# Kernel tuning notes

Hardware: AMD Instinct MI355X
Metric: run time of the kernel (lower is better)

Reference implementation:

```python
import jax, jax.numpy as jnp
import numpy as np

# --- dims (match init_kwargs) ---
B, IN_DIM, OUT_DIM, CAUSES_DIM = 4096, 512, 4096, 256
POOL = 2
N_STEPS = 10
GAMMA = 0.1
LR = 0.001  # fixed lr inside _IstaStep
S = int(np.sqrt(OUT_DIM))   # 64: side of the square code map
SP = S // POOL              # 32: pooled side
POOLED_DIM = SP * SP        # 1024: second dim of V (pool path)


def setup_inputs() -> dict:
    key = jax.random.key(0)
    k1, k2, k3 = jax.random.split(key, 3)
    inputs = jax.random.normal(k1, (B, IN_DIM), jnp.float32)
    limit = float(np.sqrt(6.0 / (OUT_DIM + IN_DIM)))  # glorot_uniform for W
    W = jax.random.uniform(k2, (OUT_DIM, IN_DIM), jnp.float32, -limit, limit)
    # pool_flag=True -> V ~ U(0, 1) with shape (causes_dim, pooled_dim)
    V = jax.random.uniform(k3, (CAUSES_DIM, POOLED_DIM), jnp.float32, 0.0, 1.0)
    return {"inputs": inputs, "W": W, "V": V}


def _soft_threshold(x, t):
    # _proxOp: max(x - t, 0) + min(x + t, 0)
    return jnp.maximum(x - t, 0.0) + jnp.minimum(x + t, 0.0)


def reference(inputs, W, V):
    Bn = inputs.shape[0]
    x0 = jnp.zeros((Bn, OUT_DIM), inputs.dtype)
    u0 = jnp.full((Bn, CAUSES_DIM), 0.1, inputs.dtype)   # zeros + 0.1
    rec0 = jnp.zeros((Bn, IN_DIM), inputs.dtype)

    def step(carry, _):
        x, u, _rec = carry
        outputs = x @ W                                   # [B, IN_DIM], linear activation
        # NOTE: original uses (1 + exp(-z)) * 0.5 (not a true sigmoid) — keep faithful
        causes = (1.0 + jnp.exp(-(u @ V))) * 0.5          # [B, POOLED_DIM]
        # nearest-neighbor upsample of the pooled cause map back to the code map
        causes_up = jnp.repeat(
            jnp.repeat(causes.reshape(Bn, SP, SP), POOL, axis=1), POOL, axis=2
        ).reshape(Bn, OUT_DIM)                            # [B, OUT_DIM]
        # T.grad(sum((inputs - x@W)^2), x) = 2 * (x@W - inputs) @ W.T
        grad_x = 2.0 * (outputs - inputs) @ W.T           # [B, OUT_DIM]
        # prior=0 in _get_output, so the _proxInnov branch is dead code
        x_new = jax.lax.stop_gradient(                    # disconnected_grad
            _soft_threshold(x - LR * grad_x, LR * GAMMA * causes_up))
        # 2x2 max pool over the square code map
        x_pool = x_new.reshape(Bn, SP, POOL, SP, POOL).max(axis=(2, 4)).reshape(Bn, POOLED_DIM)
        # T.grad(sum(causes(u) * x_pool * gamma), u): d causes/dz = -0.5*exp(-z)
        dcauses = -0.5 * jnp.exp(-(u @ V))                # [B, POOLED_DIM]
        grad_u = (dcauses * x_pool * GAMMA) @ V.T         # [B, CAUSES_DIM]
        u_new = jax.lax.stop_gradient(
            _soft_threshold(u - LR * grad_u, LR * GAMMA / 10.0))
        return (x_new, u_new, outputs), None

    (x, u, rec), _ = jax.lax.scan(step, (x0, u0, rec0), None, length=N_STEPS)
    # return_mode='rec': reconstruction computed in the last step (from x_{T-1})
    return rec
```

## Files before the change

kernel.cpp:

```cpp
#include <hip/hip_runtime.h>
#include <math.h>


#define NB 4096
#define IN_DIM 512
#define OUT_DIM 4096
#define CAUSES_DIM 256
#define POOLED_DIM 1024

typedef __attribute__((ext_vector_type(8))) short short8;
typedef __attribute__((ext_vector_type(4))) float f32x4;

static constexpr float LR = 0.001f;
static constexpr float GAMMA = 0.1f;

enum { EP_R = 0, EP_OUT, EP_CAUSES, EP_XUP, EP_XUP_LAST, EP_UUP };

__device__ __forceinline__ float softthr(float v, float t) {
    return fmaxf(v - t, 0.0f) + fminf(v + t, 0.0f);
}
__device__ __forceinline__ unsigned short f2bf(float f) {
    unsigned int u = __builtin_bit_cast(unsigned int, f);
    u = (u + 0x7fffu + ((u >> 16) & 1u)) >> 16;
    return (unsigned short)u;
}
__device__ __forceinline__ float bf2f(unsigned short h) {
    return __builtin_bit_cast(float, (unsigned int)h << 16);
}
__device__ __forceinline__ void gload_lds16(const unsigned short* g, unsigned short* l) {
    __builtin_amdgcn_global_load_lds(
        (const __attribute__((address_space(1))) void*)g,
        (__attribute__((address_space(3))) void*)l, 16, 0, 0);
}

template<int BM, int BN, int N, int K, int EP>
__global__ __launch_bounds__(256)
void gemm_bf16(const unsigned short* __restrict__ A, const unsigned short* __restrict__ B,
               const float* __restrict__ auxf,
               const unsigned short* __restrict__ cbf,
               const unsigned short* __restrict__ dcbf,
               void* __restrict__ out0, void* __restrict__ out1)
{
    constexpr int WM = BM / 2, WN = BN / 2;
    constexpr int FM = WM / 16, FN = WN / 16;
    constexpr int NK = K / 64;
    constexpr int NX = N / BN;
    constexpr int NWG = (NB / BM) * NX;
    constexpr bool POOLF = (EP == EP_XUP);
    constexpr int TILE = (BM + BN) * 64;
    constexpr int XS_SHORTS = 128 * 130;
    constexpr int LDS_SHORTS =
        (POOLF && XS_SHORTS > 2 * TILE) ? XS_SHORTS : 2 * TILE;
    __shared__ unsigned short lds[LDS_SHORTS];
    unsigned short* A0 = lds;
    unsigned short* B0 = lds + BM * 64;
    unsigned short* A1 = lds + TILE;
    unsigned short* B1 = lds + TILE + BM * 64;
    unsigned short* xs = lds;

    const int t    = threadIdx.x;
    const int lane = t & 63, wid = t >> 6;
    const int l15  = lane & 15, l7 = lane & 7, g = lane >> 4;
    const int work = ((blockIdx.x & 7) * (NWG / 8)) + (blockIdx.x >> 3);
    const int bn = work % NX, bm = work / NX;
    const int m0 = bm * BM, n0 = bn * BN;
    const int wm0 = (wid >> 1) * WM, wn0 = (wid & 1) * WN;

    f32x4 acc[FM][FN];
#pragma unroll
    for (int fi = 0; fi < FM; fi++)
#pragma unroll
        for (int fj = 0; fj < FN; fj++) acc[fi][fj] = (f32x4){0.f, 0.f, 0.f, 0.f};

    auto stage = [&](unsigned short* As, unsigned short* Bs, int k0) {
#pragma unroll
        for (int j = 0; j < BM / 32; j++) {
            const int idx = j * 256 + t;
            const int row = idx >> 3;
            const int sl  = (idx & 7) ^ (row & 7);
            gload_lds16(A + (size_t)(m0 + row) * K + k0 + sl * 8,
                        As + (size_t)(idx & ~63) * 8);
        }
#pragma unroll
        for (int j = 0; j < BN / 32; j++) {
            const int idx = j * 256 + t;
            const int row = idx >> 3;
            const int sl  = (idx & 7) ^ (row & 7);
            gload_lds16(B + (size_t)(n0 + row) * K + k0 + sl * 8,
                        Bs + (size_t)(idx & ~63) * 8);
        }
    };
    auto compute = [&](const unsigned short* As, const unsigned short* Bs) {
#pragma unroll
        for (int ks = 0; ks < 2; ks++) {
            const int so = (((ks * 4) + g) ^ l7) * 8;
            short8 af[FM], bfv[FN];
#pragma unroll
            for (int fi = 0; fi < FM; fi++)
                af[fi] = *(const short8*)&As[(wm0 + fi * 16 + l15) * 64 + so];
#pragma unroll
            for (int fj = 0; fj < FN; fj++)
                bfv[fj] = *(const short8*)&Bs[(wn0 + fj * 16 + l15) * 64 + so];
#pragma unroll
            for (int fi = 0; fi < FM; fi++)
#pragma unroll
                for (int fj = 0; fj < FN; fj++)
                    acc[fi][fj] = __builtin_amdgcn_mfma_f32_16x16x32_bf16(
                        af[fi], bfv[fj], acc[fi][fj], 0, 0, 0);
        }
    };

    stage(A0, B0, 0);
    __syncthreads();
#pragma unroll 1
    for (int kt = 0; kt < NK; kt += 2) {
        stage(A1, B1, (kt + 1) * 64);
        compute(A0, B0);
        __syncthreads();
        if (kt + 2 < NK) stage(A0, B0, (kt + 2) * 64);
        compute(A1, B1);
        __syncthreads();
    }

#pragma unroll
    for (int fi = 0; fi < FM; fi++) {
#pragma unroll
        for (int fj = 0; fj < FN; fj++) {
#pragma unroll
            for (int r = 0; r < 4; r++) {
                const int row = m0 + wm0 + fi * 16 + g * 4 + r;
                const int col = n0 + wn0 + fj * 16 + l15;
                const float v = acc[fi][fj][r];
                if (EP == EP_R) {
                    ((unsigned short*)out0)[(size_t)row * N + col] =
                        f2bf(v - auxf[(size_t)row * N + col]);
                } else if (EP == EP_OUT) {
                    ((float*)out0)[(size_t)row * N + col] = v;
                } else if (EP == EP_CAUSES) {
                    const float e = expf(-v);
                    ((unsigned short*)out0)[(size_t)row * N + col] = f2bf(0.5f + 0.5f * e);
                    ((unsigned short*)out1)[(size_t)row * N + col] = f2bf(-0.5f * e);
                } else if (EP == EP_XUP || EP == EP_XUP_LAST) {
                    const int pcol = (col & 63) >> 1;
                    const float cz = bf2f(cbf[(size_t)row * POOLED_DIM + bn * 32 + pcol]);
                    unsigned short* xbf = (unsigned short*)out0;
                    const size_t idx = (size_t)row * OUT_DIM + col;
                    const float xold = bf2f(xbf[idx]);
                    const float xv = softthr(xold - 2.0f * LR * v, LR * GAMMA * cz);
                    const unsigned short xq = f2bf(xv);
                    xbf[idx] = xq;
                    if (POOLF) {
                        const int rloc = wm0 + fi * 16 + g * 4 + r;
                        const int cloc = wn0 + fj * 16 + l15;
                        xs[rloc * 130 + cloc] = xq;
                    }
                } else {
                    float* up = (float*)out0;
                    const size_t idx = (size_t)row * CAUSES_DIM + col;
                    const float uv = softthr(up[idx] - LR * v, LR * GAMMA * 0.1f);
                    up[idx] = uv;
                    ((unsigned short*)out1)[idx] = f2bf(uv);
                }
            }
        }
    }

    if (POOLF) {
        __syncthreads();
        const int prow = t & 127;
        const int half = t >> 7;
        const size_t gp = (size_t)(m0 + prow) * POOLED_DIM + bn * 32 + half * 16;
        short8 dc0 = *(const short8*)&dcbf[gp];
        short8 dc1 = *(const short8*)&dcbf[gp + 8];
        unsigned short res[16];
#pragma unroll
        for (int i = 0; i < 16; i++) {
            const int pc = half * 16 + i;
            const unsigned short* xr = &xs[prow * 130 + 2 * pc];
            const float mx = fmaxf(fmaxf(bf2f(xr[0]), bf2f(xr[1])),
                                   fmaxf(bf2f(xr[64]), bf2f(xr[65])));
            const float dcv = bf2f((unsigned short)(i < 8 ? dc0[i] : dc1[i - 8]));
            res[i] = f2bf(dcv * mx * GAMMA);
        }
        unsigned short* gbf = (unsigned short*)out1;
        *(short8*)&gbf[gp]     = *(const short8*)&res[0];
        *(short8*)&gbf[gp + 8] = *(const short8*)&res[8];
    }
}

__global__ void cast_bf16_k(const float* __restrict__ in, unsigned short* __restrict__ out,
                            int n4, int neg)
{
    const int i = blockIdx.x * 256 + threadIdx.x;
    if (i >= n4) return;
    float4 v = ((const float4*)in)[i];
    if (neg) { v.x = -v.x; v.y = -v.y; v.z = -v.z; v.w = -v.w; }
    union { unsigned short s[4]; unsigned long long u; } p;
    p.s[0] = f2bf(v.x); p.s[1] = f2bf(v.y); p.s[2] = f2bf(v.z); p.s[3] = f2bf(v.w);
    ((unsigned long long*)out)[i] = p.u;
}

__global__ __launch_bounds__(256)
void transpose_cast_k(const float* __restrict__ in, unsigned short* __restrict__ out,
                      int R, int C)
{
    __shared__ float tile[32][33];
    const int bx = blockIdx.x * 32, by = blockIdx.y * 32;
    const int tx = threadIdx.x % 32, ty = threadIdx.x / 32;
#pragma unroll
    for (int i = 0; i < 32; i += 8)
        tile[ty + i][tx] = in[(size_t)(by + ty + i) * C + bx + tx];
    __syncthreads();
#pragma unroll
    for (int i = 0; i < 32; i += 8)
        out[(size_t)(bx + ty + i) * R + by + tx] = f2bf(tile[tx][ty + i]);
}

__global__ void fill_zero_u16(unsigned short* __restrict__ p, size_t n8) {
    for (size_t i = (size_t)blockIdx.x * 256 + threadIdx.x; i < n8;
         i += (size_t)gridDim.x * 256)
        ((ulonglong2*)p)[i] = (ulonglong2){0ull, 0ull};
}

__global__ void fill_u_k(float* __restrict__ u, unsigned short* __restrict__ ubf, int n) {
    const int i = blockIdx.x * 256 + threadIdx.x;
    if (i >= n) return;
    u[i] = 0.1f;
    ubf[i] = f2bf(0.1f);
}

extern "C" void kernel_launch(void* const* d_in, const int* in_sizes, int n_in,
                              void* d_out, int out_size, void* d_ws, size_t ws_size,
                              hipStream_t stream)
{
    const float* inputs = (const float*)d_in[0];
    const float* W      = (const float*)d_in[1];
    const float* V      = (const float*)d_in[2];
    float* out = (float*)d_out;

    char* w = (char*)d_ws;
    unsigned short* xbf  = (unsigned short*)w; w += (size_t)NB * OUT_DIM * 2;
    unsigned short* Rbf  = (unsigned short*)w; w += (size_t)NB * IN_DIM * 2;
    unsigned short* cbf  = (unsigned short*)w; w += (size_t)NB * POOLED_DIM * 2;
    unsigned short* dcbf = (unsigned short*)w; w += (size_t)NB * POOLED_DIM * 2;
    unsigned short* gbf  = (unsigned short*)w; w += (size_t)NB * POOLED_DIM * 2;
    float*          u    = (float*)w;          w += (size_t)NB * CAUSES_DIM * 4;
    unsigned short* ubf  = (unsigned short*)w; w += (size_t)NB * CAUSES_DIM * 2;
    unsigned short* Wbf  = (unsigned short*)w; w += (size_t)OUT_DIM * IN_DIM * 2;
    unsigned short* WTbf = (unsigned short*)w; w += (size_t)OUT_DIM * IN_DIM * 2;
    unsigned short* Vbf  = (unsigned short*)w; w += (size_t)CAUSES_DIM * POOLED_DIM * 2;
    unsigned short* VTbf = (unsigned short*)w;

    cast_bf16_k<<<OUT_DIM * IN_DIM / 4 / 256, 256, 0, stream>>>(W, Wbf, OUT_DIM * IN_DIM / 4, 0);
    cast_bf16_k<<<CAUSES_DIM * POOLED_DIM / 4 / 256, 256, 0, stream>>>(V, Vbf, CAUSES_DIM * POOLED_DIM / 4, 0);
    transpose_cast_k<<<dim3(IN_DIM / 32, OUT_DIM / 32), 256, 0, stream>>>(W, WTbf, OUT_DIM, IN_DIM);
    transpose_cast_k<<<dim3(POOLED_DIM / 32, CAUSES_DIM / 32), 256, 0, stream>>>(V, VTbf, CAUSES_DIM, POOLED_DIM);
    fill_zero_u16<<<2048, 256, 0, stream>>>(xbf, (size_t)NB * OUT_DIM / 8);
    fill_u_k<<<NB * CAUSES_DIM / 256, 256, 0, stream>>>(u, ubf, NB * CAUSES_DIM);
    cast_bf16_k<<<NB * IN_DIM / 4 / 256, 256, 0, stream>>>(inputs, Rbf, NB * IN_DIM / 4, 1);

    for (int t = 0; t < 9; t++) {
        if (t > 0) {
            gemm_bf16<64, 64, IN_DIM, OUT_DIM, EP_R><<<512, 256, 0, stream>>>(
                xbf, WTbf, inputs, nullptr, nullptr, Rbf, nullptr);
        }
        gemm_bf16<64, 64, POOLED_DIM, CAUSES_DIM, EP_CAUSES><<<1024, 256, 0, stream>>>(
            ubf, VTbf, nullptr, nullptr, nullptr, cbf, dcbf);
        if (t < 8) {
            gemm_bf16<128, 128, OUT_DIM, IN_DIM, EP_XUP><<<1024, 256, 0, stream>>>(
                Rbf, Wbf, nullptr, cbf, dcbf, xbf, gbf);
            gemm_bf16<64, 64, CAUSES_DIM, POOLED_DIM, EP_UUP><<<256, 256, 0, stream>>>(
                gbf, Vbf, nullptr, nullptr, nullptr, u, ubf);
        } else {
            gemm_bf16<128, 128, OUT_DIM, IN_DIM, EP_XUP_LAST><<<1024, 256, 0, stream>>>(
                Rbf, Wbf, nullptr, cbf, nullptr, xbf, nullptr);
        }
    }
    gemm_bf16<64, 64, IN_DIM, OUT_DIM, EP_OUT><<<512, 256, 0, stream>>>(
        xbf, WTbf, nullptr, nullptr, nullptr, out, nullptr);
}
```

Baseline: 843.2 us.

## Fuse causes GEMM into x-update kernel and co-launch R and u-update GEMMs

Computes the u@V causes tile inside the x-update kernel, so the causes and derivative values stay in LDS and the cbf/dcbf global buffers and the separate causes launch go away. The residual GEMM and the u-update GEMM are merged into one launch that dispatches on block index, which also lets them run concurrently. The residual and output GEMMs switch to 128x64 tiles. Each x-update block now redundantly computes a 128x32 slice of u@V (K=256), and the concurrent u-update reads the x written in the same step, which matches the original ordering.

```diff
diff --git a/kernel.cpp b/kernel.cpp
--- a/kernel.cpp
+++ b/kernel.cpp
@@ -14,7 +14,7 @@
 static constexpr float LR = 0.001f;
 static constexpr float GAMMA = 0.1f;
 
-enum { EP_R = 0, EP_OUT, EP_CAUSES, EP_XUP, EP_XUP_LAST, EP_UUP };
+enum { EP_R = 0, EP_OUT, EP_UUP };
 
 __device__ __forceinline__ float softthr(float v, float t) {
     return fmaxf(v - t, 0.0f) + fminf(v + t, 0.0f);
@@ -33,35 +33,41 @@
         (__attribute__((address_space(3))) void*)l, 16, 0, 0);
 }
 
+template<int ROWS, int K>
+__device__ __forceinline__ void stage_tile(const unsigned short* __restrict__ g,
+                                           unsigned short* l, int row0, int k0, int t)
+{
+#pragma unroll
+    for (int j = 0; j < ROWS / 32; j++) {
+        const int idx = j * 256 + t;
+        const int row = idx >> 3;
+        const int sl  = (idx & 7) ^ (row & 7);
+        gload_lds16(g + (size_t)(row0 + row) * K + k0 + sl * 8,
+                    l + (size_t)(idx & ~63) * 8);
+    }
+}
+
 template<int BM, int BN, int N, int K, int EP>
-__global__ __launch_bounds__(256)
-void gemm_bf16(const unsigned short* __restrict__ A, const unsigned short* __restrict__ B,
-               const float* __restrict__ auxf,
-               const unsigned short* __restrict__ cbf,
-               const unsigned short* __restrict__ dcbf,
-               void* __restrict__ out0, void* __restrict__ out1)
+__device__ void gemm_core(unsigned short* lds, int bid,
+                          const unsigned short* __restrict__ A,
+                          const unsigned short* __restrict__ B,
+                          const float* __restrict__ auxf,
+                          void* __restrict__ out0, void* __restrict__ out1)
 {
     constexpr int WM = BM / 2, WN = BN / 2;
     constexpr int FM = WM / 16, FN = WN / 16;
-    constexpr int NK = K / 64;
-    constexpr int NX = N / BN;
+    constexpr int NK = K / 64, NX = N / BN;
     constexpr int NWG = (NB / BM) * NX;
-    constexpr bool POOLF = (EP == EP_XUP);
     constexpr int TILE = (BM + BN) * 64;
-    constexpr int XS_SHORTS = 128 * 130;
-    constexpr int LDS_SHORTS =
-        (POOLF && XS_SHORTS > 2 * TILE) ? XS_SHORTS : 2 * TILE;
-    __shared__ unsigned short lds[LDS_SHORTS];
     unsigned short* A0 = lds;
     unsigned short* B0 = lds + BM * 64;
     unsigned short* A1 = lds + TILE;
     unsigned short* B1 = lds + TILE + BM * 64;
-    unsigned short* xs = lds;
 
     const int t    = threadIdx.x;
     const int lane = t & 63, wid = t >> 6;
     const int l15  = lane & 15, l7 = lane & 7, g = lane >> 4;
-    const int work = ((blockIdx.x & 7) * (NWG / 8)) + (blockIdx.x >> 3);
+    const int work = ((bid & 7) * (NWG / 8)) + (bid >> 3);
     const int bn = work % NX, bm = work / NX;
     const int m0 = bm * BM, n0 = bn * BN;
     const int wm0 = (wid >> 1) * WM, wn0 = (wid & 1) * WN;
@@ -72,24 +78,6 @@
 #pragma unroll
         for (int fj = 0; fj < FN; fj++) acc[fi][fj] = (f32x4){0.f, 0.f, 0.f, 0.f};
 
-    auto stage = [&](unsigned short* As, unsigned short* Bs, int k0) {
-#pragma unroll
-        for (int j = 0; j < BM / 32; j++) {
-            const int idx = j * 256 + t;
-            const int row = idx >> 3;
-            const int sl  = (idx & 7) ^ (row & 7);
-            gload_lds16(A + (size_t)(m0 + row) * K + k0 + sl * 8,
-                        As + (size_t)(idx & ~63) * 8);
-        }
-#pragma unroll
-        for (int j = 0; j < BN / 32; j++) {
-            const int idx = j * 256 + t;
-            const int row = idx >> 3;
-            const int sl  = (idx & 7) ^ (row & 7);
-            gload_lds16(B + (size_t)(n0 + row) * K + k0 + sl * 8,
-                        Bs + (size_t)(idx & ~63) * 8);
-        }
-    };
     auto compute = [&](const unsigned short* As, const unsigned short* Bs) {
 #pragma unroll
         for (int ks = 0; ks < 2; ks++) {
@@ -110,14 +98,19 @@
         }
     };
 
-    stage(A0, B0, 0);
+    stage_tile<BM, K>(A, A0, m0, 0, t);
+    stage_tile<BN, K>(B, B0, n0, 0, t);
     __syncthreads();
 #pragma unroll 1
     for (int kt = 0; kt < NK; kt += 2) {
-        stage(A1, B1, (kt + 1) * 64);
+        stage_tile<BM, K>(A, A1, m0, (kt + 1) * 64, t);
+        stage_tile<BN, K>(B, B1, n0, (kt + 1) * 64, t);
         compute(A0, B0);
         __syncthreads();
-        if (kt + 2 < NK) stage(A0, B0, (kt + 2) * 64);
+        if (kt + 2 < NK) {
+            stage_tile<BM, K>(A, A0, m0, (kt + 2) * 64, t);
+            stage_tile<BN, K>(B, B0, n0, (kt + 2) * 64, t);
+        }
         compute(A1, B1);
         __syncthreads();
     }
@@ -136,24 +129,6 @@
                         f2bf(v - auxf[(size_t)row * N + col]);
                 } else if (EP == EP_OUT) {
                     ((float*)out0)[(size_t)row * N + col] = v;
-                } else if (EP == EP_CAUSES) {
-                    const float e = expf(-v);
-                    ((unsigned short*)out0)[(size_t)row * N + col] = f2bf(0.5f + 0.5f * e);
-                    ((unsigned short*)out1)[(size_t)row * N + col] = f2bf(-0.5f * e);
-                } else if (EP == EP_XUP || EP == EP_XUP_LAST) {
-                    const int pcol = (col & 63) >> 1;
-                    const float cz = bf2f(cbf[(size_t)row * POOLED_DIM + bn * 32 + pcol]);
-                    unsigned short* xbf = (unsigned short*)out0;
-                    const size_t idx = (size_t)row * OUT_DIM + col;
-                    const float xold = bf2f(xbf[idx]);
-                    const float xv = softthr(xold - 2.0f * LR * v, LR * GAMMA * cz);
-                    const unsigned short xq = f2bf(xv);
-                    xbf[idx] = xq;
-                    if (POOLF) {
-                        const int rloc = wm0 + fi * 16 + g * 4 + r;
-                        const int cloc = wn0 + fj * 16 + l15;
-                        xs[rloc * 130 + cloc] = xq;
-                    }
                 } else {
                     float* up = (float*)out0;
                     const size_t idx = (size_t)row * CAUSES_DIM + col;
@@ -164,28 +139,189 @@
             }
         }
     }
+}
+
+template<bool POOLF>
+__global__ __launch_bounds__(256)
+void xupc_kernel(const unsigned short* __restrict__ Rbf,
+                 const unsigned short* __restrict__ Wbf,
+                 const unsigned short* __restrict__ ubf,
+                 const unsigned short* __restrict__ VTbf,
+                 unsigned short* __restrict__ xbf,
+                 unsigned short* __restrict__ gbf)
+{
+    constexpr int BM = 128, BN = 128, K = IN_DIM, NK = K / 64;
+    constexpr int NX = OUT_DIM / BN, NWG = (NB / BM) * NX;
+    constexpr int TILE = (BM + BN) * 64;
+    __shared__ unsigned short lds[2 * TILE];
+    unsigned short* A0 = lds;
+    unsigned short* B0 = lds + BM * 64;
+    unsigned short* A1 = lds + TILE;
+    unsigned short* B1 = lds + TILE + BM * 64;
+    unsigned* czdc = (unsigned*)(lds + 2 * TILE - 8192);
+    unsigned short* xs = lds;
+
+    const int t    = threadIdx.x;
+    const int lane = t & 63, wid = t >> 6;
+    const int l15  = lane & 15, l7 = lane & 7, g = lane >> 4;
+    const int work = ((blockIdx.x & 7) * (NWG / 8)) + (blockIdx.x >> 3);
+    const int bn = work % NX, bm = work / NX;
+    const int m0 = bm * BM, n0 = bn * BN;
+    const int wm0 = (wid >> 1) * 64, wn0 = (wid & 1) * 64;
+
+    f32x4 acc[4][4];
+#pragma unroll
+    for (int fi = 0; fi < 4; fi++)
+#pragma unroll
+        for (int fj = 0; fj < 4; fj++) acc[fi][fj] = (f32x4){0.f, 0.f, 0.f, 0.f};
+
+    auto compute = [&](const unsigned short* As, const unsigned short* Bs) {
+#pragma unroll
+        for (int ks = 0; ks < 2; ks++) {
+            const int so = (((ks * 4) + g) ^ l7) * 8;
+            short8 af[4], bfv[4];
+#pragma unroll
+            for (int fi = 0; fi < 4; fi++)
+                af[fi] = *(const short8*)&As[(wm0 + fi * 16 + l15) * 64 + so];
+#pragma unroll
+            for (int fj = 0; fj < 4; fj++)
+                bfv[fj] = *(const short8*)&Bs[(wn0 + fj * 16 + l15) * 64 + so];
+#pragma unroll
+            for (int fi = 0; fi < 4; fi++)
+#pragma unroll
+                for (int fj = 0; fj < 4; fj++)
+                    acc[fi][fj] = __builtin_amdgcn_mfma_f32_16x16x32_bf16(
+                        af[fi], bfv[fj], acc[fi][fj], 0, 0, 0);
+        }
+    };
+
+    stage_tile<BM, K>(Rbf, A0, m0, 0, t);
+    stage_tile<BN, K>(Wbf, B0, n0, 0, t);
+    __syncthreads();
+#pragma unroll 1
+    for (int kt = 0; kt < NK; kt += 2) {
+        stage_tile<BM, K>(Rbf, A1, m0, (kt + 1) * 64, t);
+        stage_tile<BN, K>(Wbf, B1, n0, (kt + 1) * 64, t);
+        compute(A0, B0);
+        __syncthreads();
+        if (kt + 2 < NK) {
+            stage_tile<BM, K>(Rbf, A0, m0, (kt + 2) * 64, t);
+            stage_tile<BN, K>(Wbf, B0, n0, (kt + 2) * 64, t);
+        }
+        compute(A1, B1);
+        __syncthreads();
+    }
+
+    f32x4 zacc[4];
+#pragma unroll
+    for (int fi = 0; fi < 4; fi++) zacc[fi] = (f32x4){0.f, 0.f, 0.f, 0.f};
+    const int vrow0 = bn * 32;
+    auto zcomp = [&](const unsigned short* As, const unsigned short* Bs) {
+#pragma unroll
+        for (int ks = 0; ks < 2; ks++) {
+            const int so = (((ks * 4) + g) ^ l7) * 8;
+            short8 bfv = *(const short8*)&Bs[((wid & 1) * 16 + l15) * 64 + so];
+#pragma unroll
+            for (int fi = 0; fi < 4; fi++) {
+                short8 af = *(const short8*)&As[((wid >> 1) * 64 + fi * 16 + l15) * 64 + so];
+                zacc[fi] = __builtin_amdgcn_mfma_f32_16x16x32_bf16(af, bfv, zacc[fi], 0, 0, 0);
+            }
+        }
+    };
+    stage_tile<128, CAUSES_DIM>(ubf, A0, m0, 0, t);
+    stage_tile<32, CAUSES_DIM>(VTbf, B0, vrow0, 0, t);
+    __syncthreads();
+    stage_tile<128, CAUSES_DIM>(ubf, A1, m0, 64, t);
+    stage_tile<32, CAUSES_DIM>(VTbf, B1, vrow0, 64, t);
+    zcomp(A0, B0);
+    __syncthreads();
+    stage_tile<128, CAUSES_DIM>(ubf, A0, m0, 128, t);
+    stage_tile<32, CAUSES_DIM>(VTbf, B0, vrow0, 128, t);
+    zcomp(A1, B1);
+    __syncthreads();
+    stage_tile<128, CAUSES_DIM>(ubf, A1, m0, 192, t);
+    stage_tile<32, CAUSES_DIM>(VTbf, B1, vrow0, 192, t);
+    zcomp(A0, B0);
+    __syncthreads();
+    zcomp(A1, B1);
+    __syncthreads();
+
+#pragma unroll
+    for (int fi = 0; fi < 4; fi++) {
+#pragma unroll
+        for (int r = 0; r < 4; r++) {
+            const int zrow = (wid >> 1) * 64 + fi * 16 + g * 4 + r;
+            const int zcol = (wid & 1) * 16 + l15;
+            const float e = expf(-zacc[fi][r]);
+            czdc[zrow * 32 + zcol] =
+                (unsigned)f2bf(0.5f + 0.5f * e) | ((unsigned)f2bf(-0.5f * e) << 16);
+        }
+    }
+    __syncthreads();
+
+#pragma unroll
+    for (int fi = 0; fi < 4; fi++) {
+#pragma unroll
+        for (int fj = 0; fj < 4; fj++) {
+#pragma unroll
+            for (int r = 0; r < 4; r++) {
+                const int rloc = wm0 + fi * 16 + g * 4 + r;
+                const int cloc = wn0 + fj * 16 + l15;
+                const int pl = (cloc & 63) >> 1;
+                const float cz = bf2f((unsigned short)(czdc[rloc * 32 + pl] & 0xffffu));
+                const size_t idx = (size_t)(m0 + rloc) * OUT_DIM + n0 + cloc;
+                const float xv = softthr(bf2f(xbf[idx]) - 2.0f * LR * acc[fi][fj][r],
+                                         LR * GAMMA * cz);
+                const unsigned short xq = f2bf(xv);
+                xbf[idx] = xq;
+                if (POOLF) xs[rloc * 130 + cloc] = xq;
+            }
+        }
+    }
 
     if (POOLF) {
         __syncthreads();
-        const int prow = t & 127;
-        const int half = t >> 7;
-        const size_t gp = (size_t)(m0 + prow) * POOLED_DIM + bn * 32 + half * 16;
-        short8 dc0 = *(const short8*)&dcbf[gp];
-        short8 dc1 = *(const short8*)&dcbf[gp + 8];
-        unsigned short res[16];
+        const int p = t & 31;
+        const int rbase = (t >> 5) * 16;
 #pragma unroll
         for (int i = 0; i < 16; i++) {
-            const int pc = half * 16 + i;
-            const unsigned short* xr = &xs[prow * 130 + 2 * pc];
+            const int prow = rbase + i;
+            const unsigned short* xr = &xs[prow * 130 + 2 * p];
             const float mx = fmaxf(fmaxf(bf2f(xr[0]), bf2f(xr[1])),
                                    fmaxf(bf2f(xr[64]), bf2f(xr[65])));
-            const float dcv = bf2f((unsigned short)(i < 8 ? dc0[i] : dc1[i - 8]));
-            res[i] = f2bf(dcv * mx * GAMMA);
-        }
-        unsigned short* gbf = (unsigned short*)out1;
-        *(short8*)&gbf[gp]     = *(const short8*)&res[0];
-        *(short8*)&gbf[gp + 8] = *(const short8*)&res[8];
-    }
+            const float dcv = bf2f((unsigned short)(czdc[prow * 32 + p] >> 16));
+            gbf[(size_t)(m0 + prow) * POOLED_DIM + bn * 32 + p] = f2bf(dcv * mx * GAMMA);
+        }
+    }
+}
+
+__global__ __launch_bounds__(256)
+void h_uup_r_kernel(const unsigned short* __restrict__ gbf,
+                    const unsigned short* __restrict__ Vbf,
+                    float* __restrict__ u, unsigned short* __restrict__ ubf,
+                    const unsigned short* __restrict__ xbf,
+                    const unsigned short* __restrict__ WTbf,
+                    const float* __restrict__ inputs,
+                    unsigned short* __restrict__ Rbf)
+{
+    __shared__ unsigned short lds[24576];
+    if (blockIdx.x < 256) {
+        gemm_core<128, 64, IN_DIM, OUT_DIM, EP_R>(
+            lds, blockIdx.x, xbf, WTbf, inputs, Rbf, nullptr);
+    } else {
+        gemm_core<64, 64, CAUSES_DIM, POOLED_DIM, EP_UUP>(
+            lds, blockIdx.x - 256, gbf, Vbf, nullptr, u, ubf);
+    }
+}
+
+__global__ __launch_bounds__(256)
+void out_kernel(const unsigned short* __restrict__ xbf,
+                const unsigned short* __restrict__ WTbf,
+                float* __restrict__ out)
+{
+    __shared__ unsigned short lds[24576];
+    gemm_core<128, 64, IN_DIM, OUT_DIM, EP_OUT>(
+        lds, blockIdx.x, xbf, WTbf, nullptr, out, nullptr);
 }
 
 __global__ void cast_bf16_k(const float* __restrict__ in, unsigned short* __restrict__ out,
@@ -241,8 +377,6 @@
     char* w = (char*)d_ws;
     unsigned short* xbf  = (unsigned short*)w; w += (size_t)NB * OUT_DIM * 2;
     unsigned short* Rbf  = (unsigned short*)w; w += (size_t)NB * IN_DIM * 2;
-    unsigned short* cbf  = (unsigned short*)w; w += (size_t)NB * POOLED_DIM * 2;
-    unsigned short* dcbf = (unsigned short*)w; w += (size_t)NB * POOLED_DIM * 2;
     unsigned short* gbf  = (unsigned short*)w; w += (size_t)NB * POOLED_DIM * 2;
     float*          u    = (float*)w;          w += (size_t)NB * CAUSES_DIM * 4;
     unsigned short* ubf  = (unsigned short*)w; w += (size_t)NB * CAUSES_DIM * 2;
@@ -259,23 +393,10 @@
     fill_u_k<<<NB * CAUSES_DIM / 256, 256, 0, stream>>>(u, ubf, NB * CAUSES_DIM);
     cast_bf16_k<<<NB * IN_DIM / 4 / 256, 256, 0, stream>>>(inputs, Rbf, NB * IN_DIM / 4, 1);
 
-    for (int t = 0; t < 9; t++) {
-        if (t > 0) {
-            gemm_bf16<64, 64, IN_DIM, OUT_DIM, EP_R><<<512, 256, 0, stream>>>(
-                xbf, WTbf, inputs, nullptr, nullptr, Rbf, nullptr);
-        }
-        gemm_bf16<64, 64, POOLED_DIM, CAUSES_DIM, EP_CAUSES><<<1024, 256, 0, stream>>>(
-            ubf, VTbf, nullptr, nullptr, nullptr, cbf, dcbf);
-        if (t < 8) {
-            gemm_bf16<128, 128, OUT_DIM, IN_DIM, EP_XUP><<<1024, 256, 0, stream>>>(
-                Rbf, Wbf, nullptr, cbf, dcbf, xbf, gbf);
-            gemm_bf16<64, 64, CAUSES_DIM, POOLED_DIM, EP_UUP><<<256, 256, 0, stream>>>(
-                gbf, Vbf, nullptr, nullptr, nullptr, u, ubf);
-        } else {
-            gemm_bf16<128, 128, OUT_DIM, IN_DIM, EP_XUP_LAST><<<1024, 256, 0, stream>>>(
-                Rbf, Wbf, nullptr, cbf, nullptr, xbf, nullptr);
-        }
-    }
-    gemm_bf16<64, 64, IN_DIM, OUT_DIM, EP_OUT><<<512, 256, 0, stream>>>(
-        xbf, WTbf, nullptr, nullptr, nullptr, out, nullptr);
-}
+    for (int t = 0; t < 8; t++) {
+        xupc_kernel<true><<<1024, 256, 0, stream>>>(Rbf, Wbf, ubf, VTbf, xbf, gbf);
+        h_uup_r_kernel<<<512, 256, 0, stream>>>(gbf, Vbf, u, ubf, xbf, WTbf, inputs, Rbf);
+    }
+    xupc_kernel<false><<<1024, 256, 0, stream>>>(Rbf, Wbf, ubf, VTbf, xbf, gbf);
+    out_kernel<<<256, 256, 0, stream>>>(xbf, WTbf, out);
+}
```

Result: faster. 795.2 us (-5.7%).
